# Kernel tuning notes

Measured on AMD Instinct MI355X. Metric: run time of the kernel, lower is better.

Reference implementation:

```python
import jax, jax.numpy as jnp
import numpy as np

T, B, I, H, RW, RU = 512, 64, 512, 512, 64, 64
WINIT = 0.1


def setup_inputs() -> dict:
    key = jax.random.key(0)
    ks = jax.random.split(key, 12)
    u = lambda k, shape: jax.random.uniform(k, shape, jnp.float32, -WINIT, WINIT)
    return {
        "x": jax.random.normal(ks[0], (T, B, I), jnp.float32),
        "h0": jnp.zeros((B, H), jnp.float32),
        "c0": jnp.zeros((B, H), jnp.float32),
        "U_x": u(ks[1], (I, RW)),
        "U_h": u(ks[2], (H, RU)),
        "W_x": u(ks[3], (4 * H, RW)),
        "W_h": u(ks[4], (4 * H, RU)),
        "b_x": u(ks[5], (4 * H,)),
        "b_h": u(ks[6], (4 * H,)),
        "dia_x": u(ks[7], (1, I)),
        "dia_h": u(ks[8], (1, H)),
    }


def reference(x, h0, c0, U_x, U_h, W_x, W_h, b_x, b_h, dia_x, dia_h):
    Tn, Bn, In = x.shape
    Hn = h0.shape[1]
    # Per-gate diagonal correction: sum_r U[:,r] * W[gate_slice, r] -> [4, H]
    Dx = jnp.sum(U_x[None, :, :] * W_x.reshape(4, Hn, -1), axis=-1)  # (I == H)
    Dh = jnp.sum(U_h[None, :, :] * W_h.reshape(4, Hn, -1), axis=-1)
    # Pre-batch all x-side gate pre-activations across time: [T, B, 4H]
    vm_x = jnp.tile(dia_x * x, (1, 1, 4))
    lowered_x = jnp.einsum("tbi,ir,gr->tbg", x, U_x, W_x)
    refined_x = (x[:, :, None, :] * Dx).reshape(Tn, Bn, 4 * Hn)
    gx_all = vm_x + lowered_x - refined_x + b_x

    def step(carry, gx):
        h, c = carry
        vm_h = jnp.tile(dia_h * h, (1, 4))
        lowered_h = (h @ U_h) @ W_h.T
        refined_h = (h[:, None, :] * Dh).reshape(Bn, 4 * Hn)
        g = gx + vm_h + lowered_h - refined_h + b_h
        xi, xf, xo, xn = jnp.split(g, 4, axis=1)
        i = jax.nn.sigmoid(xi)
        f = jax.nn.sigmoid(xf)
        o = jax.nn.sigmoid(xo)
        n = jnp.tanh(xn)
        c = f * c + i * n
        h = o * jnp.tanh(c)
        return (h, c), h

    (h, c), outputs = jax.lax.scan(step, (h0, c0), gx_all)
    return outputs, (h, c)
```

## Files before the change

### kernel.cpp

```cpp
#include <hip/hip_runtime.h>


typedef __fp16 h2f __attribute__((ext_vector_type(2)));
typedef unsigned int u32;
typedef unsigned short u16;

__device__ __forceinline__ float dot2f(u32 a, u32 b, float c) {
#if __has_builtin(__builtin_amdgcn_fdot2)
  return __builtin_amdgcn_fdot2(__builtin_bit_cast(h2f, a),
                                __builtin_bit_cast(h2f, b), c, false);
#else
  h2f x = __builtin_bit_cast(h2f, a);
  h2f y = __builtin_bit_cast(h2f, b);
  return c + (float)x[0] * (float)y[0] + (float)x[1] * (float)y[1];
#endif
}

__device__ __forceinline__ u32 pk2(float a, float b) {
#if __has_builtin(__builtin_amdgcn_cvt_pkrtz)
  return __builtin_bit_cast(u32, __builtin_amdgcn_cvt_pkrtz(a, b));
#else
  h2f h;
  h[0] = (__fp16)a;
  h[1] = (__fp16)b;
  return __builtin_bit_cast(u32, h);
#endif
}

__device__ __forceinline__ float h2f1(u16 u) {
  return (float)__builtin_bit_cast(__fp16, u);
}
__device__ __forceinline__ u16 f2h(float f) {
  return __builtin_bit_cast(u16, (__fp16)f);
}

__device__ __forceinline__ float dpp_xor1(float v) {
#if __has_builtin(__builtin_amdgcn_mov_dpp)
  return __builtin_bit_cast(
      float, __builtin_amdgcn_mov_dpp(__builtin_bit_cast(int, v), 0xB1, 0xF,
                                      0xF, true));
#else
  return __shfl_xor(v, 1, 64);
#endif
}

__device__ __forceinline__ void lds_barrier() {
  __builtin_amdgcn_sched_barrier(0);
  asm volatile("s_waitcnt lgkmcnt(0)" ::: "memory");
  __builtin_amdgcn_s_barrier();
  __builtin_amdgcn_sched_barrier(0);
}

__global__ void k0a_pack(const float* __restrict__ Wx, const float* __restrict__ Wh,
                         const float* __restrict__ Ux, const float* __restrict__ Uh,
                         u32* __restrict__ WxP, u32* __restrict__ WhP,
                         u32* __restrict__ UxP, u32* __restrict__ UhP) {
  int idx = blockIdx.x * 256 + threadIdx.x;
  WxP[idx] = pk2(Wx[2 * idx], Wx[2 * idx + 1]);
  WhP[idx] = pk2(Wh[2 * idx], Wh[2 * idx + 1]);
  if (idx < 16384) {
    int r = idx >> 8, k2 = idx & 255;
    UxP[idx] = pk2(Ux[(2 * k2) * 64 + r], Ux[(2 * k2 + 1) * 64 + r]);
    UhP[idx] = pk2(Uh[(2 * k2) * 64 + r], Uh[(2 * k2 + 1) * 64 + r]);
  }
}

__global__ __launch_bounds__(256) void k0b_diag(
    const float* __restrict__ Ux, const float* __restrict__ Uh,
    const float* __restrict__ Wx, const float* __restrict__ Wh,
    float* __restrict__ Dx, float* __restrict__ Dh) {
  const int t = threadIdx.x;
  const int lane = t & 63;
  const int gw = blockIdx.x * 4 + (t >> 6);
  for (int i = 0; i < 16; i++) {
    int o = gw * 16 + i;
    int which = o >> 11;
    int j = o & 2047;
    int h = j & 511;
    const float* U = which ? Uh : Ux;
    const float* W = which ? Wh : Wx;
    float v = U[h * 64 + lane] * W[j * 64 + lane];
    v += __shfl_xor(v, 1);
    v += __shfl_xor(v, 2);
    v += __shfl_xor(v, 4);
    v += __shfl_xor(v, 8);
    v += __shfl_xor(v, 16);
    v += __shfl_xor(v, 32);
    if (lane == 0) (which ? Dh : Dx)[j] = v;
  }
}

__global__ __launch_bounds__(256) void k1_xu(const float* __restrict__ x,
                                             const u32* __restrict__ UxP,
                                             u32* __restrict__ xuP) {
  __shared__ alignas(16) u32 xh[8192];
  const int tid = threadIdx.x;
  const int row0 = blockIdx.x * 32;
  const float* xs = x + (size_t)row0 * 512;

#pragma unroll
  for (int i = 0; i < 16; i++) {
    int f = tid + i * 256;
    float4 v = ((const float4*)xs)[f];
    xh[f * 2] = pk2(v.x, v.y);
    xh[f * 2 + 1] = pk2(v.z, v.w);
  }
  __syncthreads();

  const int w = tid >> 6, r = tid & 63;
  const int wr0 = w * 8;
  float acc[8] = {0.f, 0.f, 0.f, 0.f, 0.f, 0.f, 0.f, 0.f};
  const u32* Ubase = UxP + r * 256;

  for (int kc = 0; kc < 32; kc++) {
    uint4 u0 = *(const uint4*)(Ubase + kc * 8);
    uint4 u1 = *(const uint4*)(Ubase + kc * 8 + 4);
#pragma unroll
    for (int row = 0; row < 8; row++) {
      const uint4* xp = (const uint4*)&xh[(wr0 + row) * 256 + kc * 8];
      uint4 a0 = xp[0], a1 = xp[1];
      float a = acc[row];
      a = dot2f(a0.x, u0.x, a);
      a = dot2f(a0.y, u0.y, a);
      a = dot2f(a0.z, u0.z, a);
      a = dot2f(a0.w, u0.w, a);
      a = dot2f(a1.x, u1.x, a);
      a = dot2f(a1.y, u1.y, a);
      a = dot2f(a1.z, u1.z, a);
      a = dot2f(a1.w, u1.w, a);
      acc[row] = a;
    }
  }
#pragma unroll
  for (int row = 0; row < 8; row++) {
    float other = __shfl_xor(acc[row], 1, 64);
    if ((r & 1) == 0) {
      xuP[(size_t)(row0 + wr0 + row) * 32 + (r >> 1)] = pk2(acc[row], other);
    }
  }
}

__global__ __launch_bounds__(512, 2) void k2_gx(
    const float* __restrict__ x, const u32* __restrict__ xuP,
    const u32* __restrict__ WxP, const float* __restrict__ Dx,
    const float* __restrict__ bx, const float* __restrict__ diax,
    u16* __restrict__ gx) {
  __shared__ alignas(16) u32 xus[2048];
  const int t = threadIdx.x;
  const int rows0 = blockIdx.x * 64;

  uint4 Wp[4][8];
#pragma unroll
  for (int g = 0; g < 4; g++) {
    const uint4* p = (const uint4*)(WxP + (size_t)(g * 512 + t) * 32);
#pragma unroll
    for (int m = 0; m < 8; m++) Wp[g][m] = p[m];
  }
  const float dia = diax[t];
  float Dg[4], bg[4];
#pragma unroll
  for (int g = 0; g < 4; g++) {
    Dg[g] = Dx[g * 512 + t];
    bg[g] = bx[g * 512 + t];
  }
#pragma unroll
  for (int i = 0; i < 4; i++) xus[t + i * 512] = xuP[(size_t)rows0 * 32 + t + i * 512];
  __syncthreads();

  ushort4* gx4 = (ushort4*)gx;
  for (int row = 0; row < 64; row++) {
    const int R = rows0 + row;
    const uint4* s = (const uint4*)(xus + row * 32);
    float xv = x[(size_t)R * 512 + t];
    float a0 = 0.f, a1 = 0.f, a2 = 0.f, a3 = 0.f;
#pragma unroll
    for (int m = 0; m < 8; m++) {
      uint4 sm = s[m];
      uint4 w0 = Wp[0][m], w1 = Wp[1][m], w2 = Wp[2][m], w3 = Wp[3][m];
      a0 = dot2f(sm.x, w0.x, a0); a0 = dot2f(sm.y, w0.y, a0);
      a0 = dot2f(sm.z, w0.z, a0); a0 = dot2f(sm.w, w0.w, a0);
      a1 = dot2f(sm.x, w1.x, a1); a1 = dot2f(sm.y, w1.y, a1);
      a1 = dot2f(sm.z, w1.z, a1); a1 = dot2f(sm.w, w1.w, a1);
      a2 = dot2f(sm.x, w2.x, a2); a2 = dot2f(sm.y, w2.y, a2);
      a2 = dot2f(sm.z, w2.z, a2); a2 = dot2f(sm.w, w2.w, a2);
      a3 = dot2f(sm.x, w3.x, a3); a3 = dot2f(sm.y, w3.y, a3);
      a3 = dot2f(sm.z, w3.z, a3); a3 = dot2f(sm.w, w3.w, a3);
    }
    ushort4 o;
    o.x = f2h(a0 + xv * (dia - Dg[0]) + bg[0]);
    o.y = f2h(a1 + xv * (dia - Dg[1]) + bg[1]);
    o.z = f2h(a2 + xv * (dia - Dg[2]) + bg[2]);
    o.w = f2h(a3 + xv * (dia - Dg[3]) + bg[3]);
    gx4[(size_t)R * 512 + t] = o;
  }
}

__global__ __launch_bounds__(512, 2) void k3_rnn(
    const u16* __restrict__ gx, const u32* __restrict__ WhP,
    const u32* __restrict__ UhP, const float* __restrict__ Dh,
    const float* __restrict__ bh, const float* __restrict__ diah,
    float* __restrict__ out) {
  __shared__ alignas(16) u32 h32[256];
  __shared__ float partial[2][8 * 68];
  __shared__ alignas(16) u32 huW[8 * 32];

  const int t = threadIdx.x;
  const int b = blockIdx.x;
  const int lane = t & 63;
  const int w = t >> 6;

  uint4 Wp[4][8];
#pragma unroll
  for (int g = 0; g < 4; g++) {
    const uint4* p = (const uint4*)(WhP + (size_t)(g * 512 + t) * 32);
#pragma unroll
    for (int m = 0; m < 8; m++) Wp[g][m] = p[m];
  }
  uint4 Up[8];
  {
    const uint4* p = (const uint4*)(UhP + lane * 256 + w * 32);
#pragma unroll
    for (int m = 0; m < 8; m++) Up[m] = p[m];
  }
  const float dia = diah[t];
  float Dg[4], bg[4];
#pragma unroll
  for (int g = 0; g < 4; g++) {
    Dg[g] = Dh[g * 512 + t];
    bg[g] = bh[g * 512 + t];
  }

  float h = 0.f, c = 0.f;
  if (t < 256) h32[t] = 0u;

  const ushort4* gx4 = (const ushort4*)gx;
  const size_t gbase = (size_t)b * 512 + t;
  float* outb = out + (size_t)b * 512 + t;

  ushort4 gcur = gx4[gbase];
  __syncthreads();

  for (int ts = 0; ts < 512; ts++) {
    int tn = ts + (ts < 511);
    ushort4 gnext = gx4[(size_t)tn * 32768 + gbase];
    float* part = partial[ts & 1];

    const uint4* hp = ((const uint4*)h32) + w * 8;
    float acA = 0.f, acB = 0.f;
#pragma unroll
    for (int m = 0; m < 8; m += 2) {
      uint4 h0 = hp[m], h1 = hp[m + 1];
      uint4 u0 = Up[m], u1 = Up[m + 1];
      acA = dot2f(h0.x, u0.x, acA); acB = dot2f(h1.x, u1.x, acB);
      acA = dot2f(h0.y, u0.y, acA); acB = dot2f(h1.y, u1.y, acB);
      acA = dot2f(h0.z, u0.z, acA); acB = dot2f(h1.z, u1.z, acB);
      acA = dot2f(h0.w, u0.w, acA); acB = dot2f(h1.w, u1.w, acB);
    }
    part[w * 68 + lane] = acA + acB;
    lds_barrier();

    float s0 = part[0 * 68 + lane] + part[1 * 68 + lane];
    float s1 = part[2 * 68 + lane] + part[3 * 68 + lane];
    float s2 = part[4 * 68 + lane] + part[5 * 68 + lane];
    float s3 = part[6 * 68 + lane] + part[7 * 68 + lane];
    float hu = (s0 + s1) + (s2 + s3);
    float huo = dpp_xor1(hu);
    if ((lane & 1) == 0) huW[w * 32 + (lane >> 1)] = pk2(hu, huo);
    const uint4* hup = ((const uint4*)huW) + w * 8;

    float a0 = 0.f, a1 = 0.f, a2 = 0.f, a3 = 0.f;
#pragma unroll
    for (int m = 0; m < 8; m++) {
      uint4 hm = hup[m];
      uint4 w0 = Wp[0][m], w1 = Wp[1][m], w2 = Wp[2][m], w3 = Wp[3][m];
      a0 = dot2f(hm.x, w0.x, a0); a1 = dot2f(hm.x, w1.x, a1);
      a2 = dot2f(hm.x, w2.x, a2); a3 = dot2f(hm.x, w3.x, a3);
      a0 = dot2f(hm.y, w0.y, a0); a1 = dot2f(hm.y, w1.y, a1);
      a2 = dot2f(hm.y, w2.y, a2); a3 = dot2f(hm.y, w3.y, a3);
      a0 = dot2f(hm.z, w0.z, a0); a1 = dot2f(hm.z, w1.z, a1);
      a2 = dot2f(hm.z, w2.z, a2); a3 = dot2f(hm.z, w3.z, a3);
      a0 = dot2f(hm.w, w0.w, a0); a1 = dot2f(hm.w, w1.w, a1);
      a2 = dot2f(hm.w, w2.w, a2); a3 = dot2f(hm.w, w3.w, a3);
    }
    float hd = h;
    float pre0 = a0 + h2f1(gcur.x) + hd * (dia - Dg[0]) + bg[0];
    float pre1 = a1 + h2f1(gcur.y) + hd * (dia - Dg[1]) + bg[1];
    float pre2 = a2 + h2f1(gcur.z) + hd * (dia - Dg[2]) + bg[2];
    float pre3 = a3 + h2f1(gcur.w) + hd * (dia - Dg[3]) + bg[3];

    float ig = 1.f / (1.f + __expf(-pre0));
    float fg = 1.f / (1.f + __expf(-pre1));
    float og = 1.f / (1.f + __expf(-pre2));
    float e2 = __expf(2.f * pre3);
    float ng = 1.f - 2.f / (e2 + 1.f);
    c = fg * c + ig * ng;
    float e2c = __expf(2.f * c);
    h = og * (1.f - 2.f / (e2c + 1.f));

    outb[(size_t)ts * 32768] = h;
    ((u16*)h32)[t] = f2h(h);
    gcur = gnext;
  }
  out[(size_t)512 * 32768 + (size_t)b * 512 + t] = h;
  out[(size_t)512 * 32768 + 32768 + (size_t)b * 512 + t] = c;
}

extern "C" void kernel_launch(void* const* d_in, const int* in_sizes, int n_in,
                              void* d_out, int out_size, void* d_ws,
                              size_t ws_size, hipStream_t stream) {
  const float* x = (const float*)d_in[0];
  const float* Ux = (const float*)d_in[3];
  const float* Uh = (const float*)d_in[4];
  const float* Wx = (const float*)d_in[5];
  const float* Wh = (const float*)d_in[6];
  const float* bx = (const float*)d_in[7];
  const float* bh = (const float*)d_in[8];
  const float* diax = (const float*)d_in[9];
  const float* diah = (const float*)d_in[10];
  float* out = (float*)d_out;

  char* ws = (char*)d_ws;
  u16* gx = (u16*)ws;
  u32* xuP = (u32*)(ws + 134217728);
  u32* WxP = (u32*)(ws + 138412032);
  u32* WhP = (u32*)(ws + 138674176);
  u32* UxP = (u32*)(ws + 138936320);
  u32* UhP = (u32*)(ws + 139001856);
  float* Dx = (float*)(ws + 139067392);
  float* Dh = (float*)(ws + 139075584);

  k0a_pack<<<256, 256, 0, stream>>>(Wx, Wh, Ux, Uh, WxP, WhP, UxP, UhP);
  k0b_diag<<<64, 256, 0, stream>>>(Ux, Uh, Wx, Wh, Dx, Dh);
  k1_xu<<<1024, 256, 0, stream>>>(x, UxP, xuP);
  k2_gx<<<512, 512, 0, stream>>>(x, xuP, WxP, Dx, bx, diax, gx);
  k3_rnn<<<64, 512, 0, stream>>>(gx, WhP, UhP, Dh, bh, diah, out);
}
```

Before: 889.1 us.

## Process two batch rows per block in recurrent kernel to reuse register weights

The recurrent LSTM kernel now assigns two batch elements to each block and halves the grid, so the Wh/Uh weights held in registers are reused for both rows. Per-step LDS buffers and the reductions are doubled, and the launch bound drops to one block per CU. This cuts redundant weight loading and barrier count per batch row, at the cost of roughly doubling per-step work on the serial critical path and using fewer CUs.

```diff
diff --git a/kernel.cpp b/kernel.cpp
--- a/kernel.cpp
+++ b/kernel.cpp
@@ -195,17 +195,17 @@
   }
 }
 
-__global__ __launch_bounds__(512, 2) void k3_rnn(
+__global__ __launch_bounds__(512, 1) void k3_rnn(
     const u16* __restrict__ gx, const u32* __restrict__ WhP,
     const u32* __restrict__ UhP, const float* __restrict__ Dh,
     const float* __restrict__ bh, const float* __restrict__ diah,
     float* __restrict__ out) {
-  __shared__ alignas(16) u32 h32[256];
-  __shared__ float partial[2][8 * 68];
-  __shared__ alignas(16) u32 huW[8 * 32];
+  __shared__ alignas(16) u32 h32[512];
+  __shared__ float partial[2][2][8 * 68];
+  __shared__ alignas(16) u32 huW[2][8 * 32];
 
   const int t = threadIdx.x;
-  const int b = blockIdx.x;
+  const int b0 = blockIdx.x * 2;
   const int lane = t & 63;
   const int w = t >> 6;
 
@@ -230,79 +230,130 @@
     bg[g] = bh[g * 512 + t];
   }
 
-  float h = 0.f, c = 0.f;
-  if (t < 256) h32[t] = 0u;
+  float h0 = 0.f, c0 = 0.f, h1 = 0.f, c1 = 0.f;
+  h32[t] = 0u;
 
   const ushort4* gx4 = (const ushort4*)gx;
-  const size_t gbase = (size_t)b * 512 + t;
-  float* outb = out + (size_t)b * 512 + t;
-
-  ushort4 gcur = gx4[gbase];
+  const size_t gbase = (size_t)b0 * 512 + t;
+  float* outb = out + (size_t)b0 * 512 + t;
+
+  ushort4 gcur0 = gx4[gbase];
+  ushort4 gcur1 = gx4[gbase + 512];
   __syncthreads();
 
   for (int ts = 0; ts < 512; ts++) {
     int tn = ts + (ts < 511);
-    ushort4 gnext = gx4[(size_t)tn * 32768 + gbase];
-    float* part = partial[ts & 1];
-
-    const uint4* hp = ((const uint4*)h32) + w * 8;
-    float acA = 0.f, acB = 0.f;
+    ushort4 gn0 = gx4[(size_t)tn * 32768 + gbase];
+    ushort4 gn1 = gx4[(size_t)tn * 32768 + gbase + 512];
+    float* part0 = partial[0][ts & 1];
+    float* part1 = partial[1][ts & 1];
+
+    const uint4* hp0 = ((const uint4*)h32) + w * 8;
+    const uint4* hp1 = ((const uint4*)h32) + 64 + w * 8;
+    float aA0 = 0.f, aB0 = 0.f, aA1 = 0.f, aB1 = 0.f;
 #pragma unroll
     for (int m = 0; m < 8; m += 2) {
-      uint4 h0 = hp[m], h1 = hp[m + 1];
+      uint4 x0 = hp0[m], x1 = hp0[m + 1];
+      uint4 y0 = hp1[m], y1 = hp1[m + 1];
       uint4 u0 = Up[m], u1 = Up[m + 1];
-      acA = dot2f(h0.x, u0.x, acA); acB = dot2f(h1.x, u1.x, acB);
-      acA = dot2f(h0.y, u0.y, acA); acB = dot2f(h1.y, u1.y, acB);
-      acA = dot2f(h0.z, u0.z, acA); acB = dot2f(h1.z, u1.z, acB);
-      acA = dot2f(h0.w, u0.w, acA); acB = dot2f(h1.w, u1.w, acB);
-    }
-    part[w * 68 + lane] = acA + acB;
+      aA0 = dot2f(x0.x, u0.x, aA0); aB0 = dot2f(x1.x, u1.x, aB0);
+      aA1 = dot2f(y0.x, u0.x, aA1); aB1 = dot2f(y1.x, u1.x, aB1);
+      aA0 = dot2f(x0.y, u0.y, aA0); aB0 = dot2f(x1.y, u1.y, aB0);
+      aA1 = dot2f(y0.y, u0.y, aA1); aB1 = dot2f(y1.y, u1.y, aB1);
+      aA0 = dot2f(x0.z, u0.z, aA0); aB0 = dot2f(x1.z, u1.z, aB0);
+      aA1 = dot2f(y0.z, u0.z, aA1); aB1 = dot2f(y1.z, u1.z, aB1);
+      aA0 = dot2f(x0.w, u0.w, aA0); aB0 = dot2f(x1.w, u1.w, aB0);
+      aA1 = dot2f(y0.w, u0.w, aA1); aB1 = dot2f(y1.w, u1.w, aB1);
+    }
+    part0[w * 68 + lane] = aA0 + aB0;
+    part1[w * 68 + lane] = aA1 + aB1;
     lds_barrier();
 
-    float s0 = part[0 * 68 + lane] + part[1 * 68 + lane];
-    float s1 = part[2 * 68 + lane] + part[3 * 68 + lane];
-    float s2 = part[4 * 68 + lane] + part[5 * 68 + lane];
-    float s3 = part[6 * 68 + lane] + part[7 * 68 + lane];
-    float hu = (s0 + s1) + (s2 + s3);
-    float huo = dpp_xor1(hu);
-    if ((lane & 1) == 0) huW[w * 32 + (lane >> 1)] = pk2(hu, huo);
-    const uint4* hup = ((const uint4*)huW) + w * 8;
-
-    float a0 = 0.f, a1 = 0.f, a2 = 0.f, a3 = 0.f;
+    float p00 = part0[0 * 68 + lane] + part0[1 * 68 + lane];
+    float p01 = part0[2 * 68 + lane] + part0[3 * 68 + lane];
+    float p02 = part0[4 * 68 + lane] + part0[5 * 68 + lane];
+    float p03 = part0[6 * 68 + lane] + part0[7 * 68 + lane];
+    float p10 = part1[0 * 68 + lane] + part1[1 * 68 + lane];
+    float p11 = part1[2 * 68 + lane] + part1[3 * 68 + lane];
+    float p12 = part1[4 * 68 + lane] + part1[5 * 68 + lane];
+    float p13 = part1[6 * 68 + lane] + part1[7 * 68 + lane];
+    float hu0 = (p00 + p01) + (p02 + p03);
+    float hu1 = (p10 + p11) + (p12 + p13);
+    float ho0 = dpp_xor1(hu0);
+    float ho1 = dpp_xor1(hu1);
+    if ((lane & 1) == 0) {
+      huW[0][w * 32 + (lane >> 1)] = pk2(hu0, ho0);
+      huW[1][w * 32 + (lane >> 1)] = pk2(hu1, ho1);
+    }
+    const uint4* hup0 = ((const uint4*)huW[0]) + w * 8;
+    const uint4* hup1 = ((const uint4*)huW[1]) + w * 8;
+
+    float a00 = 0.f, a10 = 0.f, a20 = 0.f, a30 = 0.f;
+    float a01 = 0.f, a11 = 0.f, a21 = 0.f, a31 = 0.f;
 #pragma unroll
     for (int m = 0; m < 8; m++) {
-      uint4 hm = hup[m];
+      uint4 m0 = hup0[m], m1 = hup1[m];
       uint4 w0 = Wp[0][m], w1 = Wp[1][m], w2 = Wp[2][m], w3 = Wp[3][m];
-      a0 = dot2f(hm.x, w0.x, a0); a1 = dot2f(hm.x, w1.x, a1);
-      a2 = dot2f(hm.x, w2.x, a2); a3 = dot2f(hm.x, w3.x, a3);
-      a0 = dot2f(hm.y, w0.y, a0); a1 = dot2f(hm.y, w1.y, a1);
-      a2 = dot2f(hm.y, w2.y, a2); a3 = dot2f(hm.y, w3.y, a3);
-      a0 = dot2f(hm.z, w0.z, a0); a1 = dot2f(hm.z, w1.z, a1);
-      a2 = dot2f(hm.z, w2.z, a2); a3 = dot2f(hm.z, w3.z, a3);
-      a0 = dot2f(hm.w, w0.w, a0); a1 = dot2f(hm.w, w1.w, a1);
-      a2 = dot2f(hm.w, w2.w, a2); a3 = dot2f(hm.w, w3.w, a3);
-    }
-    float hd = h;
-    float pre0 = a0 + h2f1(gcur.x) + hd * (dia - Dg[0]) + bg[0];
-    float pre1 = a1 + h2f1(gcur.y) + hd * (dia - Dg[1]) + bg[1];
-    float pre2 = a2 + h2f1(gcur.z) + hd * (dia - Dg[2]) + bg[2];
-    float pre3 = a3 + h2f1(gcur.w) + hd * (dia - Dg[3]) + bg[3];
-
-    float ig = 1.f / (1.f + __expf(-pre0));
-    float fg = 1.f / (1.f + __expf(-pre1));
-    float og = 1.f / (1.f + __expf(-pre2));
-    float e2 = __expf(2.f * pre3);
-    float ng = 1.f - 2.f / (e2 + 1.f);
-    c = fg * c + ig * ng;
-    float e2c = __expf(2.f * c);
-    h = og * (1.f - 2.f / (e2c + 1.f));
-
-    outb[(size_t)ts * 32768] = h;
-    ((u16*)h32)[t] = f2h(h);
-    gcur = gnext;
-  }
-  out[(size_t)512 * 32768 + (size_t)b * 512 + t] = h;
-  out[(size_t)512 * 32768 + 32768 + (size_t)b * 512 + t] = c;
+      a00 = dot2f(m0.x, w0.x, a00); a01 = dot2f(m1.x, w0.x, a01);
+      a10 = dot2f(m0.x, w1.x, a10); a11 = dot2f(m1.x, w1.x, a11);
+      a20 = dot2f(m0.x, w2.x, a20); a21 = dot2f(m1.x, w2.x, a21);
+      a30 = dot2f(m0.x, w3.x, a30); a31 = dot2f(m1.x, w3.x, a31);
+      a00 = dot2f(m0.y, w0.y, a00); a01 = dot2f(m1.y, w0.y, a01);
+      a10 = dot2f(m0.y, w1.y, a10); a11 = dot2f(m1.y, w1.y, a11);
+      a20 = dot2f(m0.y, w2.y, a20); a21 = dot2f(m1.y, w2.y, a21);
+      a30 = dot2f(m0.y, w3.y, a30); a31 = dot2f(m1.y, w3.y, a31);
+      a00 = dot2f(m0.z, w0.z, a00); a01 = dot2f(m1.z, w0.z, a01);
+      a10 = dot2f(m0.z, w1.z, a10); a11 = dot2f(m1.z, w1.z, a11);
+      a20 = dot2f(m0.z, w2.z, a20); a21 = dot2f(m1.z, w2.z, a21);
+      a30 = dot2f(m0.z, w3.z, a30); a31 = dot2f(m1.z, w3.z, a31);
+      a00 = dot2f(m0.w, w0.w, a00); a01 = dot2f(m1.w, w0.w, a01);
+      a10 = dot2f(m0.w, w1.w, a10); a11 = dot2f(m1.w, w1.w, a11);
+      a20 = dot2f(m0.w, w2.w, a20); a21 = dot2f(m1.w, w2.w, a21);
+      a30 = dot2f(m0.w, w3.w, a30); a31 = dot2f(m1.w, w3.w, a31);
+    }
+
+    {
+      float hd = h0;
+      float pre0 = a00 + h2f1(gcur0.x) + hd * (dia - Dg[0]) + bg[0];
+      float pre1 = a10 + h2f1(gcur0.y) + hd * (dia - Dg[1]) + bg[1];
+      float pre2 = a20 + h2f1(gcur0.z) + hd * (dia - Dg[2]) + bg[2];
+      float pre3 = a30 + h2f1(gcur0.w) + hd * (dia - Dg[3]) + bg[3];
+      float ig = 1.f / (1.f + __expf(-pre0));
+      float fg = 1.f / (1.f + __expf(-pre1));
+      float og = 1.f / (1.f + __expf(-pre2));
+      float e2 = __expf(2.f * pre3);
+      float ng = 1.f - 2.f / (e2 + 1.f);
+      c0 = fg * c0 + ig * ng;
+      float e2c = __expf(2.f * c0);
+      h0 = og * (1.f - 2.f / (e2c + 1.f));
+    }
+    {
+      float hd = h1;
+      float pre0 = a01 + h2f1(gcur1.x) + hd * (dia - Dg[0]) + bg[0];
+      float pre1 = a11 + h2f1(gcur1.y) + hd * (dia - Dg[1]) + bg[1];
+      float pre2 = a21 + h2f1(gcur1.z) + hd * (dia - Dg[2]) + bg[2];
+      float pre3 = a31 + h2f1(gcur1.w) + hd * (dia - Dg[3]) + bg[3];
+      float ig = 1.f / (1.f + __expf(-pre0));
+      float fg = 1.f / (1.f + __expf(-pre1));
+      float og = 1.f / (1.f + __expf(-pre2));
+      float e2 = __expf(2.f * pre3);
+      float ng = 1.f - 2.f / (e2 + 1.f);
+      c1 = fg * c1 + ig * ng;
+      float e2c = __expf(2.f * c1);
+      h1 = og * (1.f - 2.f / (e2c + 1.f));
+    }
+
+    outb[(size_t)ts * 32768] = h0;
+    outb[(size_t)ts * 32768 + 512] = h1;
+    ((u16*)h32)[t] = f2h(h0);
+    ((u16*)h32)[512 + t] = f2h(h1);
+    gcur0 = gn0;
+    gcur1 = gn1;
+  }
+  out[(size_t)512 * 32768 + (size_t)b0 * 512 + t] = h0;
+  out[(size_t)512 * 32768 + (size_t)b0 * 512 + 512 + t] = h1;
+  out[(size_t)512 * 32768 + 32768 + (size_t)b0 * 512 + t] = c0;
+  out[(size_t)512 * 32768 + 32768 + (size_t)b0 * 512 + 512 + t] = c1;
 }
 
 extern "C" void kernel_launch(void* const* d_in, const int* in_sizes, int n_in,
@@ -333,5 +384,5 @@
   k0b_diag<<<64, 256, 0, stream>>>(Ux, Uh, Wx, Wh, Dx, Dh);
   k1_xu<<<1024, 256, 0, stream>>>(x, UxP, xuP);
   k2_gx<<<512, 512, 0, stream>>>(x, xuP, WxP, Dx, bx, diax, gx);
-  k3_rnn<<<64, 512, 0, stream>>>(gx, WhP, UhP, Dh, bh, diah, out);
-}
+  k3_rnn<<<32, 512, 0, stream>>>(gx, WhP, UhP, Dh, bh, diah, out);
+}
```

Measured after the change: 1.434 ms. 61.3% more time.
